# Optimization experiments

Measured on AMD Instinct MI355X. Metric: run time of the kernel, lower is better.

## Reference

```python
import jax, jax.numpy as jnp
import numpy as np

B, NI, D, P, R = 32, 1024, 1024, 1000, 3  # batch, patches, d_model, pool_size, agg rounds


def setup_inputs() -> dict:
    key = jax.random.key(0)
    ks = jax.random.split(key, 12)
    w = lambda k, shape: jax.random.normal(k, shape, jnp.float32) * 0.02
    return {
        "att_feats": jax.random.normal(ks[0], (B, NI, D), jnp.float32),
        "fc_feats": jax.random.normal(ks[1], (B, D), jnp.float32),
        "pool": jax.random.normal(ks[2], (P, D), jnp.float32),
        "W_agg": w(ks[3], (R, D, D)),          # stacked agg projections (no bias)
        "Wq": w(ks[4], (D, D)), "bq": jnp.zeros((D,), jnp.float32),
        "Wk": w(ks[5], (D, D)), "bk": jnp.zeros((D,), jnp.float32),
        "Wv": w(ks[6], (D, D)), "bv": jnp.zeros((D,), jnp.float32),
        "Wc": w(ks[7], (D, D)), "bc": jnp.zeros((D,), jnp.float32),
        "Wg": w(ks[8], (2 * D,)), "bg": jnp.asarray(-1.0, jnp.float32),  # gate bias init -1
        "residual_scale": jnp.asarray(0.1, jnp.float32),
    }


def reference(att_feats, fc_feats, pool, W_agg, Wq, bq, Wk, bk, Wv, bv, Wc, bc, Wg, bg, residual_scale):
    d = att_feats.shape[-1]
    scale = 1.0 / jnp.sqrt(jnp.asarray(d, att_feats.dtype))
    v_hat = fc_feats  # fc dim == d_model path

    # Aggregate attention: R rounds over normality pool, averaged (Eq. 4-6)
    q_all = jnp.einsum('bd,rod->rbo', v_hat, W_agg)            # [R,B,D]
    scores = jnp.einsum('rbo,po->rbp', q_all, pool) * scale    # [R,B,P]
    weights = jax.nn.softmax(scores, axis=-1)
    v_agg = jnp.einsum('rbp,pd->bd', weights, pool) / R        # [B,D]

    # Differentiate attention (Eq. 7-10)
    q = v_hat @ Wq.T + bq
    k = v_agg @ Wk.T + bk
    v = v_agg @ Wv.T + bv
    sim = jnp.sum(q * k, axis=-1, keepdims=True) * scale       # [B,1]
    v_common = jax.nn.sigmoid(sim) * v
    v_diff = jax.nn.relu((v_hat - v_common) @ Wc.T + bc)       # [B,D] (dropout = identity, eval)

    # Gated residual; split gate weight to avoid materializing the concat
    Wg1, Wg2 = Wg[:d], Wg[d:]
    g = jax.nn.sigmoid(att_feats @ Wg1 + (v_diff @ Wg2)[:, None] + bg)  # [B,NI]
    return att_feats + residual_scale * g[..., None] * v_diff[:, None, :]
```

## Files before the change

kernel.cpp:

```cpp
#include <hip/hip_runtime.h>

#define D 1024
#define B 32
#define NI 1024
#define PP 1000
#define R 3
#define SPLITS 8
#define VS 8
#define BK 32
#define KT (D / SPLITS / BK)
#define PAD 34

typedef float f32x4_t __attribute__((ext_vector_type(4)));

__device__ __forceinline__ void nt_store4(float* p, float4 v) {
    f32x4_t x = {v.x, v.y, v.z, v.w};
    __builtin_nontemporal_store(x, (f32x4_t*)p);
}

__device__ __forceinline__ float wred(float x) {
    #pragma unroll
    for (int off = 32; off; off >>= 1) x += __shfl_xor(x, off, 64);
    return x;
}
__device__ __forceinline__ float wmax(float x) {
    #pragma unroll
    for (int off = 32; off; off >>= 1) x = fmaxf(x, __shfl_xor(x, off, 64));
    return x;
}

template<int NXS>
__device__ __forceinline__ void gemm_core(
        const float* __restrict__ A, int mbase, int Mrows,
        const float* __restrict__ Xb, int xrstride, size_t xss,
        int kc0, float acc[4][4]) {
    __shared__ float Ws[128][PAD];
    __shared__ float Xs[32][PAD];
    const int t = threadIdx.x;
    const int ty = t >> 3, tx = t & 7;
    const int m0 = 4 * ty, b0 = 4 * tx;
    const int lrow = t >> 3, lq = t & 7;

    #pragma unroll
    for (int i = 0; i < 4; ++i)
        #pragma unroll
        for (int j = 0; j < 4; ++j) acc[i][j] = 0.f;

    for (int kt = 0; kt < KT; ++kt) {
        const int kc = kc0 + kt * BK;
        #pragma unroll
        for (int rr = 0; rr < 4; ++rr) {
            const int row = lrow + 32 * rr;
            float4 v = make_float4(0.f, 0.f, 0.f, 0.f);
            if (mbase + row < Mrows)
                v = *(const float4*)(A + (size_t)(mbase + row) * D + kc + 4 * lq);
            *(float2*)&Ws[row][4 * lq]     = make_float2(v.x, v.y);
            *(float2*)&Ws[row][4 * lq + 2] = make_float2(v.z, v.w);
        }
        {
            const float* xp = Xb + (size_t)lrow * xrstride + kc + 4 * lq;
            float4 v = *(const float4*)xp;
            #pragma unroll
            for (int s = 1; s < NXS; ++s) {
                float4 w = *(const float4*)(xp + (size_t)s * xss);
                v.x += w.x; v.y += w.y; v.z += w.z; v.w += w.w;
            }
            *(float2*)&Xs[lrow][4 * lq]     = make_float2(v.x, v.y);
            *(float2*)&Xs[lrow][4 * lq + 2] = make_float2(v.z, v.w);
        }
        __syncthreads();
        #pragma unroll
        for (int kp = 0; kp < 16; ++kp) {
            float2 wv[4], xv[4];
            #pragma unroll
            for (int i = 0; i < 4; ++i) wv[i] = *(const float2*)&Ws[m0 + i][2 * kp];
            #pragma unroll
            for (int j = 0; j < 4; ++j) xv[j] = *(const float2*)&Xs[b0 + j][2 * kp];
            #pragma unroll
            for (int i = 0; i < 4; ++i)
                #pragma unroll
                for (int j = 0; j < 4; ++j) {
                    acc[i][j] += wv[i].x * xv[j].x;
                    acc[i][j] += wv[i].y * xv[j].y;
                }
        }
        __syncthreads();
    }
}

__global__ __launch_bounds__(256) void gemm_k1(const float* __restrict__ Wagg,
        const float* __restrict__ fc, float* __restrict__ Cp) {
    const int mb = blockIdx.x, s = blockIdx.y;
    const int mbase = mb * 128;
    float acc[4][4];
    gemm_core<1>(Wagg, mbase, R * D, fc, D, 0, s * 128, acc);
    const int t = threadIdx.x, ty = t >> 3, tx = t & 7;
    const int m = mbase + 4 * ty;
    #pragma unroll
    for (int j = 0; j < 4; ++j) {
        float* cp = Cp + ((size_t)(s * B) + 4 * tx + j) * (R * D) + m;
        *(float4*)cp = make_float4(acc[0][j], acc[1][j], acc[2][j], acc[3][j]);
    }
}

__global__ __launch_bounds__(256) void gemm_k2(const float* __restrict__ pool,
        const float* __restrict__ qallp, float* __restrict__ Cp) {
    const int mb = blockIdx.x, s = blockIdx.y, r = blockIdx.z;
    const int mbase = mb * 128;
    float acc[4][4];
    gemm_core<SPLITS>(pool, mbase, PP, qallp + r * D, R * D, (size_t)B * R * D,
                      s * 128, acc);
    const int t = threadIdx.x, ty = t >> 3, tx = t & 7;
    const int m = mbase + 4 * ty;
    if (m >= PP) return;
    #pragma unroll
    for (int j = 0; j < 4; ++j) {
        float* cp = Cp + ((size_t)((s * R + r) * B) + 4 * tx + j) * D + m;
        *(float4*)cp = make_float4(acc[0][j], acc[1][j], acc[2][j], acc[3][j]);
    }
}

__global__ __launch_bounds__(256) void gemm_k5(const float* __restrict__ Wq,
        const float* __restrict__ Wk, const float* __restrict__ Wv,
        const float* __restrict__ fc, const float* __restrict__ vaggp,
        float* __restrict__ Cp) {
    const int mb = blockIdx.x, s = blockIdx.y, z = blockIdx.z;
    const int mbase = mb * 128;
    float acc[4][4];
    if (z == 0)
        gemm_core<1>(Wq, mbase, D, fc, D, 0, s * 128, acc);
    else
        gemm_core<VS>((z == 1) ? Wk : Wv, mbase, D, vaggp, D, (size_t)B * D,
                      s * 128, acc);
    const int t = threadIdx.x, ty = t >> 3, tx = t & 7;
    const int m = mbase + 4 * ty;
    #pragma unroll
    for (int j = 0; j < 4; ++j) {
        float* cp = Cp + ((size_t)((s * R + z) * B) + 4 * tx + j) * D + m;
        *(float4*)cp = make_float4(acc[0][j], acc[1][j], acc[2][j], acc[3][j]);
    }
}

__global__ __launch_bounds__(256) void gemm_k7(const float* __restrict__ Wc,
        const float* __restrict__ u, float* __restrict__ Cp) {
    const int mb = blockIdx.x, s = blockIdx.y;
    const int mbase = mb * 128;
    float acc[4][4];
    gemm_core<1>(Wc, mbase, D, u, D, 0, s * 128, acc);
    const int t = threadIdx.x, ty = t >> 3, tx = t & 7;
    const int m = mbase + 4 * ty;
    #pragma unroll
    for (int j = 0; j < 4; ++j) {
        float* cp = Cp + ((size_t)(s * B) + 4 * tx + j) * D + m;
        *(float4*)cp = make_float4(acc[0][j], acc[1][j], acc[2][j], acc[3][j]);
    }
}

__global__ __launch_bounds__(256) void k3_wbar(const float* __restrict__ scp,
        float* __restrict__ wbar) {
    const int b = blockIdx.x;
    const int t = threadIdx.x, w = t >> 6, lane = t & 63;
    __shared__ float red[8];
    float wb[4] = {0.f, 0.f, 0.f, 0.f};
    for (int r = 0; r < R; ++r) {
        float v[4];
        float mx = -1e30f;
        #pragma unroll
        for (int i = 0; i < 4; ++i) {
            const int p = t + 256 * i;
            float x = -1e30f;
            if (p < PP) {
                x = 0.f;
                #pragma unroll
                for (int s = 0; s < SPLITS; ++s)
                    x += scp[((size_t)((s * R + r) * B) + b) * D + p];
                x *= 0.03125f;
            }
            v[i] = x;
            mx = fmaxf(mx, x);
        }
        mx = wmax(mx);
        if (lane == 0) red[w] = mx;
        __syncthreads();
        mx = fmaxf(fmaxf(red[0], red[1]), fmaxf(red[2], red[3]));
        float e[4], sum = 0.f;
        #pragma unroll
        for (int i = 0; i < 4; ++i) {
            const int p = t + 256 * i;
            e[i] = (p < PP) ? __expf(v[i] - mx) : 0.f;
            sum += e[i];
        }
        sum = wred(sum);
        if (lane == 0) red[4 + w] = sum;
        __syncthreads();
        const float inv = 1.f / (red[4] + red[5] + red[6] + red[7]);
        #pragma unroll
        for (int i = 0; i < 4; ++i) wb[i] += e[i] * inv;
        __syncthreads();
    }
    #pragma unroll
    for (int i = 0; i < 4; ++i) {
        const int p = t + 256 * i;
        wbar[(size_t)b * 1024 + p] = wb[i] * (1.f / 3.f);
    }
}

__global__ __launch_bounds__(256) void k4_vagg(const float* __restrict__ wbar,
        const float* __restrict__ pool, float* __restrict__ vaggp) {
    const int db = blockIdx.x, ps = blockIdx.y;
    __shared__ float Ps[32][132];
    __shared__ float Wbt[32][36];
    const int t = threadIdx.x;
    const int ty = t >> 3, tx = t & 7;
    float acc[4][4];
    #pragma unroll
    for (int i = 0; i < 4; ++i)
        #pragma unroll
        for (int j = 0; j < 4; ++j) acc[i][j] = 0.f;

    for (int pt = 0; pt < 4; ++pt) {
        const int p0 = ps * 128 + pt * 32;
        {
            const int prow = t >> 5, qc = t & 31;
            #pragma unroll
            for (int rr = 0; rr < 4; ++rr) {
                const int pr = prow + 8 * rr;
                float4 v = make_float4(0.f, 0.f, 0.f, 0.f);
                if (p0 + pr < PP)
                    v = *(const float4*)(pool + (size_t)(p0 + pr) * D + db * 128 + 4 * qc);
                *(float4*)&Ps[pr][4 * qc] = v;
            }
        }
        {
            const int bb = t >> 3, q = t & 7;
            float4 v = *(const float4*)(wbar + (size_t)bb * 1024 + p0 + 4 * q);
            Wbt[4 * q + 0][bb] = v.x; Wbt[4 * q + 1][bb] = v.y;
            Wbt[4 * q + 2][bb] = v.z; Wbt[4 * q + 3][bb] = v.w;
        }
        __syncthreads();
        #pragma unroll
        for (int pg = 0; pg < 8; ++pg) {
            #pragma unroll
            for (int pp = 0; pp < 4; ++pp) {
                const int p = 4 * pg + pp;
                float4 xv = *(const float4*)&Ps[p][4 * ty];
                float4 wv = *(const float4*)&Wbt[p][4 * tx];
                const float xs[4] = {xv.x, xv.y, xv.z, xv.w};
                const float wsv[4] = {wv.x, wv.y, wv.z, wv.w};
                #pragma unroll
                for (int i = 0; i < 4; ++i)
                    #pragma unroll
                    for (int j = 0; j < 4; ++j)
                        acc[i][j] += xs[i] * wsv[j];
            }
        }
        __syncthreads();
    }
    const int dbase = db * 128 + 4 * ty;
    #pragma unroll
    for (int j = 0; j < 4; ++j) {
        float* op = vaggp + ((size_t)ps * B + 4 * tx + j) * D + dbase;
        *(float4*)op = make_float4(acc[0][j], acc[1][j], acc[2][j], acc[3][j]);
    }
}

__global__ __launch_bounds__(256) void k6_u(const float* __restrict__ qkvp,
        const float* __restrict__ bq, const float* __restrict__ bk,
        const float* __restrict__ bv, const float* __restrict__ vhat,
        float* __restrict__ u) {
    const int b = blockIdx.x;
    const int t = threadIdx.x, w = t >> 6, lane = t & 63;
    const int d = 4 * t;
    float4 qv = *(const float4*)(bq + d);
    float4 kv = *(const float4*)(bk + d);
    #pragma unroll
    for (int s = 0; s < SPLITS; ++s) {
        float4 a = *(const float4*)(qkvp + ((size_t)((s * R + 0) * B) + b) * D + d);
        float4 c = *(const float4*)(qkvp + ((size_t)((s * R + 1) * B) + b) * D + d);
        qv.x += a.x; qv.y += a.y; qv.z += a.z; qv.w += a.w;
        kv.x += c.x; kv.y += c.y; kv.z += c.z; kv.w += c.w;
    }
    float local = qv.x * kv.x + qv.y * kv.y + qv.z * kv.z + qv.w * kv.w;
    local = wred(local);
    __shared__ float red[4];
    if (lane == 0) red[w] = local;
    __syncthreads();
    const float sim = (red[0] + red[1] + red[2] + red[3]) * 0.03125f;
    const float sig = 1.f / (1.f + __expf(-sim));
    float4 vv = *(const float4*)(bv + d);
    #pragma unroll
    for (int s = 0; s < SPLITS; ++s) {
        float4 c = *(const float4*)(qkvp + ((size_t)((s * R + 2) * B) + b) * D + d);
        vv.x += c.x; vv.y += c.y; vv.z += c.z; vv.w += c.w;
    }
    const float4 vh = *(const float4*)(vhat + (size_t)b * D + d);
    float4 o;
    o.x = vh.x - sig * vv.x; o.y = vh.y - sig * vv.y;
    o.z = vh.z - sig * vv.z; o.w = vh.w - sig * vv.w;
    *(float4*)(u + (size_t)b * D + d) = o;
}

__global__ __launch_bounds__(256) void k8_cb(const float* __restrict__ vdp,
        const float* __restrict__ bc, const float* __restrict__ Wg,
        const float* __restrict__ bg, float* __restrict__ vdiff,
        float* __restrict__ cb) {
    const int b = blockIdx.x;
    const int t = threadIdx.x, w = t >> 6, lane = t & 63;
    const int d = 4 * t;
    float4 a = *(const float4*)(bc + d);
    #pragma unroll
    for (int s = 0; s < SPLITS; ++s) {
        float4 c = *(const float4*)(vdp + ((size_t)(s * B) + b) * D + d);
        a.x += c.x; a.y += c.y; a.z += c.z; a.w += c.w;
    }
    a.x = fmaxf(a.x, 0.f); a.y = fmaxf(a.y, 0.f);
    a.z = fmaxf(a.z, 0.f); a.w = fmaxf(a.w, 0.f);
    *(float4*)(vdiff + (size_t)b * D + d) = a;
    const float4 g2 = *(const float4*)(Wg + D + d);
    float local = a.x * g2.x + a.y * g2.y + a.z * g2.z + a.w * g2.w;
    local = wred(local);
    __shared__ float red[4];
    if (lane == 0) red[w] = local;
    __syncthreads();
    if (t == 0) cb[b] = red[0] + red[1] + red[2] + red[3] + bg[0];
}

__global__ __launch_bounds__(256, 2) void k9_main(const float* __restrict__ att,
        const float* __restrict__ Wg, const float* __restrict__ cb,
        const float* __restrict__ vdiff, const float* __restrict__ rs_p,
        float* __restrict__ out) {
    __shared__ float vds[1024];
    const int t = threadIdx.x;
    const int b = blockIdx.x >> 5;
    *(float4*)&vds[4 * t] = *(const float4*)(vdiff + (size_t)b * D + 4 * t);
    __syncthreads();
    const int w = t >> 6, lane = t & 63;
    float4 g[4];
    #pragma unroll
    for (int kk = 0; kk < 4; ++kk)
        g[kk] = *(const float4*)(Wg + 4 * lane + 256 * kk);
    const float rsv = rs_p[0];
    const float cbb = cb[b];
    const size_t row0 = (size_t)b * NI + (size_t)(blockIdx.x & 31) * 32 + w * 8;
    const float* ap = att + row0 * D;
    float* op = out + row0 * D;

    float4 cur[8], nxt[8];
    #pragma unroll
    for (int q = 0; q < 8; ++q)
        cur[q] = *(const float4*)(ap + (size_t)(q >> 2) * D + 4 * lane + 256 * (q & 3));

    #pragma unroll
    for (int it = 0; it < 4; ++it) {
        if (it < 3) {
            const float* apn = ap + (size_t)(2 * it + 2) * D;
            #pragma unroll
            for (int q = 0; q < 8; ++q)
                nxt[q] = *(const float4*)(apn + (size_t)(q >> 2) * D + 4 * lane + 256 * (q & 3));
        }
        float acc0 = 0.f, acc1 = 0.f;
        #pragma unroll
        for (int kk = 0; kk < 4; ++kk) {
            acc0 += cur[kk].x * g[kk].x + cur[kk].y * g[kk].y +
                    cur[kk].z * g[kk].z + cur[kk].w * g[kk].w;
            acc1 += cur[4 + kk].x * g[kk].x + cur[4 + kk].y * g[kk].y +
                    cur[4 + kk].z * g[kk].z + cur[4 + kk].w * g[kk].w;
        }
        #pragma unroll
        for (int off = 32; off; off >>= 1) {
            acc0 += __shfl_xor(acc0, off, 64);
            acc1 += __shfl_xor(acc1, off, 64);
        }
        const float grs0 = rsv / (1.f + __expf(-(acc0 + cbb)));
        const float grs1 = rsv / (1.f + __expf(-(acc1 + cbb)));
        float* op0 = op + (size_t)(2 * it) * D;
        #pragma unroll
        for (int kk = 0; kk < 4; ++kk) {
            const int col = 4 * lane + 256 * kk;
            const float4 vd = *(const float4*)&vds[col];
            float4 o0, o1;
            o0.x = cur[kk].x + grs0 * vd.x; o0.y = cur[kk].y + grs0 * vd.y;
            o0.z = cur[kk].z + grs0 * vd.z; o0.w = cur[kk].w + grs0 * vd.w;
            o1.x = cur[4 + kk].x + grs1 * vd.x; o1.y = cur[4 + kk].y + grs1 * vd.y;
            o1.z = cur[4 + kk].z + grs1 * vd.z; o1.w = cur[4 + kk].w + grs1 * vd.w;
            nt_store4(op0 + col, o0);
            nt_store4(op0 + D + col, o1);
        }
        if (it < 3) {
            #pragma unroll
            for (int q = 0; q < 8; ++q) cur[q] = nxt[q];
        }
    }
}

extern "C" void kernel_launch(void* const* d_in, const int* in_sizes, int n_in,
                              void* d_out, int out_size, void* d_ws, size_t ws_size,
                              hipStream_t stream) {
    const float* att  = (const float*)d_in[0];
    const float* fc   = (const float*)d_in[1];
    const float* pool = (const float*)d_in[2];
    const float* Wagg = (const float*)d_in[3];
    const float* Wq   = (const float*)d_in[4];
    const float* bq   = (const float*)d_in[5];
    const float* Wk   = (const float*)d_in[6];
    const float* bk   = (const float*)d_in[7];
    const float* Wv   = (const float*)d_in[8];
    const float* bv   = (const float*)d_in[9];
    const float* Wc   = (const float*)d_in[10];
    const float* bc   = (const float*)d_in[11];
    const float* Wg   = (const float*)d_in[12];
    const float* bg   = (const float*)d_in[13];
    const float* rs   = (const float*)d_in[14];
    float* out = (float*)d_out;

    float* ws = (float*)d_ws;
    float* qallp = ws;
    float* scp   = qallp + (size_t)SPLITS * B * R * D;
    float* wbar  = scp + (size_t)SPLITS * R * B * D;
    float* vaggp = wbar + (size_t)B * 1024;
    float* qkvp  = vaggp + (size_t)VS * B * D;
    float* ub    = qkvp + (size_t)SPLITS * R * B * D;
    float* vdp   = ub + (size_t)B * D;
    float* vdiff = vdp + (size_t)SPLITS * B * D;
    float* cbuf  = vdiff + (size_t)B * D;

    gemm_k1<<<dim3(24, SPLITS), 256, 0, stream>>>(Wagg, fc, qallp);
    gemm_k2<<<dim3(8, SPLITS, R), 256, 0, stream>>>(pool, qallp, scp);
    k3_wbar<<<B, 256, 0, stream>>>(scp, wbar);
    k4_vagg<<<dim3(8, VS), 256, 0, stream>>>(wbar, pool, vaggp);
    gemm_k5<<<dim3(8, SPLITS, R), 256, 0, stream>>>(Wq, Wk, Wv, fc, vaggp, qkvp);
    k6_u<<<B, 256, 0, stream>>>(qkvp, bq, bk, bv, fc, ub);
    gemm_k7<<<dim3(8, SPLITS), 256, 0, stream>>>(Wc, ub, vdp);
    k8_cb<<<B, 256, 0, stream>>>(vdp, bc, Wg, bg, vdiff, cbuf);
    k9_main<<<B * 32, 256, 0, stream>>>(att, Wg, cbuf, vdiff, rs, out);
}
```

Before: 131.2 us.

## Fuse eight dependent small kernels into one cooperative kernel with grid syncs

Replaces the chain of eight small GEMM and reduction launches with a single cooperative kernel of 192 blocks that runs each stage in turn, separated by grid-wide barriers. It also moves the Wq projection so it runs alongside the v_agg stage, since the two do not depend on each other. The aim is to remove per-launch overhead and the gaps between dependent launches. The cost is grid.sync barriers, idle blocks in the narrow stages, and a fixed grid size that must fit co-resident on the device.

```diff
diff --git a/kernel.cpp b/kernel.cpp
--- a/kernel.cpp
+++ b/kernel.cpp
@@ -1,4 +1,7 @@
 #include <hip/hip_runtime.h>
+#include <hip/hip_cooperative_groups.h>
+
+namespace cg = cooperative_groups;
 
 #define D 1024
 #define B 32
@@ -30,12 +33,10 @@
 }
 
 template<int NXS>
-__device__ __forceinline__ void gemm_core(
+__device__ __forceinline__ void gemm_core_l(
         const float* __restrict__ A, int mbase, int Mrows,
         const float* __restrict__ Xb, int xrstride, size_t xss,
-        int kc0, float acc[4][4]) {
-    __shared__ float Ws[128][PAD];
-    __shared__ float Xs[32][PAD];
+        int kc0, float acc[4][4], float (*Ws)[PAD], float (*Xs)[PAD]) {
     const int t = threadIdx.x;
     const int ty = t >> 3, tx = t & 7;
     const int m0 = 4 * ty, b0 = 4 * tx;
@@ -88,241 +89,252 @@
     }
 }
 
-__global__ __launch_bounds__(256) void gemm_k1(const float* __restrict__ Wagg,
-        const float* __restrict__ fc, float* __restrict__ Cp) {
-    const int mb = blockIdx.x, s = blockIdx.y;
-    const int mbase = mb * 128;
-    float acc[4][4];
-    gemm_core<1>(Wagg, mbase, R * D, fc, D, 0, s * 128, acc);
-    const int t = threadIdx.x, ty = t >> 3, tx = t & 7;
-    const int m = mbase + 4 * ty;
-    #pragma unroll
-    for (int j = 0; j < 4; ++j) {
-        float* cp = Cp + ((size_t)(s * B) + 4 * tx + j) * (R * D) + m;
-        *(float4*)cp = make_float4(acc[0][j], acc[1][j], acc[2][j], acc[3][j]);
-    }
-}
-
-__global__ __launch_bounds__(256) void gemm_k2(const float* __restrict__ pool,
-        const float* __restrict__ qallp, float* __restrict__ Cp) {
-    const int mb = blockIdx.x, s = blockIdx.y, r = blockIdx.z;
-    const int mbase = mb * 128;
-    float acc[4][4];
-    gemm_core<SPLITS>(pool, mbase, PP, qallp + r * D, R * D, (size_t)B * R * D,
-                      s * 128, acc);
-    const int t = threadIdx.x, ty = t >> 3, tx = t & 7;
-    const int m = mbase + 4 * ty;
-    if (m >= PP) return;
-    #pragma unroll
-    for (int j = 0; j < 4; ++j) {
-        float* cp = Cp + ((size_t)((s * R + r) * B) + 4 * tx + j) * D + m;
-        *(float4*)cp = make_float4(acc[0][j], acc[1][j], acc[2][j], acc[3][j]);
-    }
-}
-
-__global__ __launch_bounds__(256) void gemm_k5(const float* __restrict__ Wq,
+__global__ __launch_bounds__(256) void chain_all(
+        const float* __restrict__ fc, const float* __restrict__ pool,
+        const float* __restrict__ Wagg, const float* __restrict__ Wq,
         const float* __restrict__ Wk, const float* __restrict__ Wv,
-        const float* __restrict__ fc, const float* __restrict__ vaggp,
-        float* __restrict__ Cp) {
-    const int mb = blockIdx.x, s = blockIdx.y, z = blockIdx.z;
-    const int mbase = mb * 128;
-    float acc[4][4];
-    if (z == 0)
-        gemm_core<1>(Wq, mbase, D, fc, D, 0, s * 128, acc);
-    else
-        gemm_core<VS>((z == 1) ? Wk : Wv, mbase, D, vaggp, D, (size_t)B * D,
-                      s * 128, acc);
-    const int t = threadIdx.x, ty = t >> 3, tx = t & 7;
-    const int m = mbase + 4 * ty;
-    #pragma unroll
-    for (int j = 0; j < 4; ++j) {
-        float* cp = Cp + ((size_t)((s * R + z) * B) + 4 * tx + j) * D + m;
-        *(float4*)cp = make_float4(acc[0][j], acc[1][j], acc[2][j], acc[3][j]);
-    }
-}
-
-__global__ __launch_bounds__(256) void gemm_k7(const float* __restrict__ Wc,
-        const float* __restrict__ u, float* __restrict__ Cp) {
-    const int mb = blockIdx.x, s = blockIdx.y;
-    const int mbase = mb * 128;
-    float acc[4][4];
-    gemm_core<1>(Wc, mbase, D, u, D, 0, s * 128, acc);
-    const int t = threadIdx.x, ty = t >> 3, tx = t & 7;
-    const int m = mbase + 4 * ty;
-    #pragma unroll
-    for (int j = 0; j < 4; ++j) {
-        float* cp = Cp + ((size_t)(s * B) + 4 * tx + j) * D + m;
-        *(float4*)cp = make_float4(acc[0][j], acc[1][j], acc[2][j], acc[3][j]);
-    }
-}
-
-__global__ __launch_bounds__(256) void k3_wbar(const float* __restrict__ scp,
-        float* __restrict__ wbar) {
-    const int b = blockIdx.x;
-    const int t = threadIdx.x, w = t >> 6, lane = t & 63;
-    __shared__ float red[8];
-    float wb[4] = {0.f, 0.f, 0.f, 0.f};
-    for (int r = 0; r < R; ++r) {
-        float v[4];
-        float mx = -1e30f;
-        #pragma unroll
-        for (int i = 0; i < 4; ++i) {
-            const int p = t + 256 * i;
-            float x = -1e30f;
-            if (p < PP) {
-                x = 0.f;
+        const float* __restrict__ bq, const float* __restrict__ bk,
+        const float* __restrict__ bv, const float* __restrict__ Wc,
+        const float* __restrict__ bc, const float* __restrict__ Wg,
+        const float* __restrict__ bg,
+        float* __restrict__ qallp, float* __restrict__ scp,
+        float* __restrict__ wbar, float* __restrict__ vaggp,
+        float* __restrict__ qkvp, float* __restrict__ ub,
+        float* __restrict__ vdp, float* __restrict__ vdiff,
+        float* __restrict__ cb) {
+    cg::grid_group grid = cg::this_grid();
+    const int bid = blockIdx.x;
+    const int t = threadIdx.x;
+    __shared__ float lds_raw[160 * PAD];
+    __shared__ float red8[8];
+    float (*Ws)[PAD] = (float(*)[PAD])lds_raw;
+    float (*Xs)[PAD] = (float(*)[PAD])&lds_raw[128 * PAD];
+    const int ty = t >> 3, tx = t & 7;
+
+    {
+        const int mb = bid / SPLITS, s = bid % SPLITS;
+        float acc[4][4];
+        gemm_core_l<1>(Wagg, mb * 128, R * D, fc, D, 0, s * 128, acc, Ws, Xs);
+        const int m = mb * 128 + 4 * ty;
+        #pragma unroll
+        for (int j = 0; j < 4; ++j) {
+            float* cp = qallp + ((size_t)(s * B) + 4 * tx + j) * (R * D) + m;
+            *(float4*)cp = make_float4(acc[0][j], acc[1][j], acc[2][j], acc[3][j]);
+        }
+    }
+    grid.sync();
+
+    {
+        const int r = bid / 64, rem = bid % 64;
+        const int s = rem >> 3, mb = rem & 7;
+        float acc[4][4];
+        gemm_core_l<SPLITS>(pool, mb * 128, PP, qallp + r * D, R * D,
+                            (size_t)B * R * D, s * 128, acc, Ws, Xs);
+        const int m = mb * 128 + 4 * ty;
+        if (m < PP) {
+            #pragma unroll
+            for (int j = 0; j < 4; ++j) {
+                float* cp = scp + ((size_t)((s * R + r) * B) + 4 * tx + j) * D + m;
+                *(float4*)cp = make_float4(acc[0][j], acc[1][j], acc[2][j], acc[3][j]);
+            }
+        }
+    }
+    grid.sync();
+
+    if (bid < B) {
+        const int b = bid;
+        const int w = t >> 6, lane = t & 63;
+        float wb[4] = {0.f, 0.f, 0.f, 0.f};
+        for (int r = 0; r < R; ++r) {
+            float v[4];
+            float mx = -1e30f;
+            #pragma unroll
+            for (int i = 0; i < 4; ++i) {
+                const int p = t + 256 * i;
+                float x = -1e30f;
+                if (p < PP) {
+                    x = 0.f;
+                    #pragma unroll
+                    for (int s = 0; s < SPLITS; ++s)
+                        x += scp[((size_t)((s * R + r) * B) + b) * D + p];
+                    x *= 0.03125f;
+                }
+                v[i] = x;
+                mx = fmaxf(mx, x);
+            }
+            mx = wmax(mx);
+            if (lane == 0) red8[w] = mx;
+            __syncthreads();
+            mx = fmaxf(fmaxf(red8[0], red8[1]), fmaxf(red8[2], red8[3]));
+            float e[4], sum = 0.f;
+            #pragma unroll
+            for (int i = 0; i < 4; ++i) {
+                const int p = t + 256 * i;
+                e[i] = (p < PP) ? __expf(v[i] - mx) : 0.f;
+                sum += e[i];
+            }
+            sum = wred(sum);
+            if (lane == 0) red8[4 + w] = sum;
+            __syncthreads();
+            const float inv = 1.f / (red8[4] + red8[5] + red8[6] + red8[7]);
+            #pragma unroll
+            for (int i = 0; i < 4; ++i) wb[i] += e[i] * inv;
+            __syncthreads();
+        }
+        #pragma unroll
+        for (int i = 0; i < 4; ++i)
+            wbar[(size_t)b * 1024 + t + 256 * i] = wb[i] * (1.f / 3.f);
+    }
+    grid.sync();
+
+    if (bid < 64) {
+        const int db = bid & 7, ps = bid >> 3;
+        float (*Ps)[132] = (float(*)[132])lds_raw;
+        float (*Wbt)[36] = (float(*)[36])&lds_raw[32 * 132];
+        float acc[4][4];
+        #pragma unroll
+        for (int i = 0; i < 4; ++i)
+            #pragma unroll
+            for (int j = 0; j < 4; ++j) acc[i][j] = 0.f;
+        for (int pt = 0; pt < 4; ++pt) {
+            const int p0 = ps * 128 + pt * 32;
+            {
+                const int prow = t >> 5, qc = t & 31;
                 #pragma unroll
-                for (int s = 0; s < SPLITS; ++s)
-                    x += scp[((size_t)((s * R + r) * B) + b) * D + p];
-                x *= 0.03125f;
-            }
-            v[i] = x;
-            mx = fmaxf(mx, x);
-        }
-        mx = wmax(mx);
-        if (lane == 0) red[w] = mx;
+                for (int rr = 0; rr < 4; ++rr) {
+                    const int pr = prow + 8 * rr;
+                    float4 v = make_float4(0.f, 0.f, 0.f, 0.f);
+                    if (p0 + pr < PP)
+                        v = *(const float4*)(pool + (size_t)(p0 + pr) * D + db * 128 + 4 * qc);
+                    *(float4*)&Ps[pr][4 * qc] = v;
+                }
+            }
+            {
+                const int bb = t >> 3, q = t & 7;
+                float4 v = *(const float4*)(wbar + (size_t)bb * 1024 + p0 + 4 * q);
+                Wbt[4 * q + 0][bb] = v.x; Wbt[4 * q + 1][bb] = v.y;
+                Wbt[4 * q + 2][bb] = v.z; Wbt[4 * q + 3][bb] = v.w;
+            }
+            __syncthreads();
+            #pragma unroll
+            for (int pg = 0; pg < 8; ++pg) {
+                #pragma unroll
+                for (int pp = 0; pp < 4; ++pp) {
+                    const int p = 4 * pg + pp;
+                    float4 xv = *(const float4*)&Ps[p][4 * ty];
+                    float4 wv = *(const float4*)&Wbt[p][4 * tx];
+                    const float xsv[4] = {xv.x, xv.y, xv.z, xv.w};
+                    const float wsv[4] = {wv.x, wv.y, wv.z, wv.w};
+                    #pragma unroll
+                    for (int i = 0; i < 4; ++i)
+                        #pragma unroll
+                        for (int j = 0; j < 4; ++j)
+                            acc[i][j] += xsv[i] * wsv[j];
+                }
+            }
+            __syncthreads();
+        }
+        const int dbase = db * 128 + 4 * ty;
+        #pragma unroll
+        for (int j = 0; j < 4; ++j) {
+            float* op = vaggp + ((size_t)ps * B + 4 * tx + j) * D + dbase;
+            *(float4*)op = make_float4(acc[0][j], acc[1][j], acc[2][j], acc[3][j]);
+        }
+    } else if (bid < 128) {
+        const int i0 = bid - 64;
+        const int mb = i0 & 7, s = i0 >> 3;
+        float acc[4][4];
+        gemm_core_l<1>(Wq, mb * 128, D, fc, D, 0, s * 128, acc, Ws, Xs);
+        const int m = mb * 128 + 4 * ty;
+        #pragma unroll
+        for (int j = 0; j < 4; ++j) {
+            float* cp = qkvp + ((size_t)((s * R + 0) * B) + 4 * tx + j) * D + m;
+            *(float4*)cp = make_float4(acc[0][j], acc[1][j], acc[2][j], acc[3][j]);
+        }
+    }
+    grid.sync();
+
+    if (bid < 128) {
+        const int z = bid >> 6, rem = bid & 63;
+        const int s = rem >> 3, mb = rem & 7;
+        float acc[4][4];
+        gemm_core_l<VS>((z == 0) ? Wk : Wv, mb * 128, D, vaggp, D,
+                        (size_t)B * D, s * 128, acc, Ws, Xs);
+        const int m = mb * 128 + 4 * ty;
+        #pragma unroll
+        for (int j = 0; j < 4; ++j) {
+            float* cp = qkvp + ((size_t)((s * R + z + 1) * B) + 4 * tx + j) * D + m;
+            *(float4*)cp = make_float4(acc[0][j], acc[1][j], acc[2][j], acc[3][j]);
+        }
+    }
+    grid.sync();
+
+    if (bid < B) {
+        const int b = bid;
+        const int w = t >> 6, lane = t & 63;
+        const int d = 4 * t;
+        float4 qv = *(const float4*)(bq + d);
+        float4 kv = *(const float4*)(bk + d);
+        #pragma unroll
+        for (int s = 0; s < SPLITS; ++s) {
+            float4 a = *(const float4*)(qkvp + ((size_t)((s * R + 0) * B) + b) * D + d);
+            float4 c = *(const float4*)(qkvp + ((size_t)((s * R + 1) * B) + b) * D + d);
+            qv.x += a.x; qv.y += a.y; qv.z += a.z; qv.w += a.w;
+            kv.x += c.x; kv.y += c.y; kv.z += c.z; kv.w += c.w;
+        }
+        float local = qv.x * kv.x + qv.y * kv.y + qv.z * kv.z + qv.w * kv.w;
+        local = wred(local);
+        if (lane == 0) red8[w] = local;
         __syncthreads();
-        mx = fmaxf(fmaxf(red[0], red[1]), fmaxf(red[2], red[3]));
-        float e[4], sum = 0.f;
-        #pragma unroll
-        for (int i = 0; i < 4; ++i) {
-            const int p = t + 256 * i;
-            e[i] = (p < PP) ? __expf(v[i] - mx) : 0.f;
-            sum += e[i];
-        }
-        sum = wred(sum);
-        if (lane == 0) red[4 + w] = sum;
+        const float sim = (red8[0] + red8[1] + red8[2] + red8[3]) * 0.03125f;
+        const float sig = 1.f / (1.f + __expf(-sim));
+        float4 vv = *(const float4*)(bv + d);
+        #pragma unroll
+        for (int s = 0; s < SPLITS; ++s) {
+            float4 c = *(const float4*)(qkvp + ((size_t)((s * R + 2) * B) + b) * D + d);
+            vv.x += c.x; vv.y += c.y; vv.z += c.z; vv.w += c.w;
+        }
+        const float4 vh = *(const float4*)(fc + (size_t)b * D + d);
+        float4 o;
+        o.x = vh.x - sig * vv.x; o.y = vh.y - sig * vv.y;
+        o.z = vh.z - sig * vv.z; o.w = vh.w - sig * vv.w;
+        *(float4*)(ub + (size_t)b * D + d) = o;
+    }
+    grid.sync();
+
+    if (bid < 64) {
+        const int s = bid >> 3, mb = bid & 7;
+        float acc[4][4];
+        gemm_core_l<1>(Wc, mb * 128, D, ub, D, 0, s * 128, acc, Ws, Xs);
+        const int m = mb * 128 + 4 * ty;
+        #pragma unroll
+        for (int j = 0; j < 4; ++j) {
+            float* cp = vdp + ((size_t)(s * B) + 4 * tx + j) * D + m;
+            *(float4*)cp = make_float4(acc[0][j], acc[1][j], acc[2][j], acc[3][j]);
+        }
+    }
+    grid.sync();
+
+    if (bid < B) {
+        const int b = bid;
+        const int w = t >> 6, lane = t & 63;
+        const int d = 4 * t;
+        float4 a = *(const float4*)(bc + d);
+        #pragma unroll
+        for (int s = 0; s < SPLITS; ++s) {
+            float4 c = *(const float4*)(vdp + ((size_t)(s * B) + b) * D + d);
+            a.x += c.x; a.y += c.y; a.z += c.z; a.w += c.w;
+        }
+        a.x = fmaxf(a.x, 0.f); a.y = fmaxf(a.y, 0.f);
+        a.z = fmaxf(a.z, 0.f); a.w = fmaxf(a.w, 0.f);
+        *(float4*)(vdiff + (size_t)b * D + d) = a;
+        const float4 g2 = *(const float4*)(Wg + D + d);
+        float local = a.x * g2.x + a.y * g2.y + a.z * g2.z + a.w * g2.w;
+        local = wred(local);
+        if (lane == 0) red8[w] = local;
         __syncthreads();
-        const float inv = 1.f / (red[4] + red[5] + red[6] + red[7]);
-        #pragma unroll
-        for (int i = 0; i < 4; ++i) wb[i] += e[i] * inv;
-        __syncthreads();
-    }
-    #pragma unroll
-    for (int i = 0; i < 4; ++i) {
-        const int p = t + 256 * i;
-        wbar[(size_t)b * 1024 + p] = wb[i] * (1.f / 3.f);
-    }
-}
-
-__global__ __launch_bounds__(256) void k4_vagg(const float* __restrict__ wbar,
-        const float* __restrict__ pool, float* __restrict__ vaggp) {
-    const int db = blockIdx.x, ps = blockIdx.y;
-    __shared__ float Ps[32][132];
-    __shared__ float Wbt[32][36];
-    const int t = threadIdx.x;
-    const int ty = t >> 3, tx = t & 7;
-    float acc[4][4];
-    #pragma unroll
-    for (int i = 0; i < 4; ++i)
-        #pragma unroll
-        for (int j = 0; j < 4; ++j) acc[i][j] = 0.f;
-
-    for (int pt = 0; pt < 4; ++pt) {
-        const int p0 = ps * 128 + pt * 32;
-        {
-            const int prow = t >> 5, qc = t & 31;
-            #pragma unroll
-            for (int rr = 0; rr < 4; ++rr) {
-                const int pr = prow + 8 * rr;
-                float4 v = make_float4(0.f, 0.f, 0.f, 0.f);
-                if (p0 + pr < PP)
-                    v = *(const float4*)(pool + (size_t)(p0 + pr) * D + db * 128 + 4 * qc);
-                *(float4*)&Ps[pr][4 * qc] = v;
-            }
-        }
-        {
-            const int bb = t >> 3, q = t & 7;
-            float4 v = *(const float4*)(wbar + (size_t)bb * 1024 + p0 + 4 * q);
-            Wbt[4 * q + 0][bb] = v.x; Wbt[4 * q + 1][bb] = v.y;
-            Wbt[4 * q + 2][bb] = v.z; Wbt[4 * q + 3][bb] = v.w;
-        }
-        __syncthreads();
-        #pragma unroll
-        for (int pg = 0; pg < 8; ++pg) {
-            #pragma unroll
-            for (int pp = 0; pp < 4; ++pp) {
-                const int p = 4 * pg + pp;
-                float4 xv = *(const float4*)&Ps[p][4 * ty];
-                float4 wv = *(const float4*)&Wbt[p][4 * tx];
-                const float xs[4] = {xv.x, xv.y, xv.z, xv.w};
-                const float wsv[4] = {wv.x, wv.y, wv.z, wv.w};
-                #pragma unroll
-                for (int i = 0; i < 4; ++i)
-                    #pragma unroll
-                    for (int j = 0; j < 4; ++j)
-                        acc[i][j] += xs[i] * wsv[j];
-            }
-        }
-        __syncthreads();
-    }
-    const int dbase = db * 128 + 4 * ty;
-    #pragma unroll
-    for (int j = 0; j < 4; ++j) {
-        float* op = vaggp + ((size_t)ps * B + 4 * tx + j) * D + dbase;
-        *(float4*)op = make_float4(acc[0][j], acc[1][j], acc[2][j], acc[3][j]);
-    }
-}
-
-__global__ __launch_bounds__(256) void k6_u(const float* __restrict__ qkvp,
-        const float* __restrict__ bq, const float* __restrict__ bk,
-        const float* __restrict__ bv, const float* __restrict__ vhat,
-        float* __restrict__ u) {
-    const int b = blockIdx.x;
-    const int t = threadIdx.x, w = t >> 6, lane = t & 63;
-    const int d = 4 * t;
-    float4 qv = *(const float4*)(bq + d);
-    float4 kv = *(const float4*)(bk + d);
-    #pragma unroll
-    for (int s = 0; s < SPLITS; ++s) {
-        float4 a = *(const float4*)(qkvp + ((size_t)((s * R + 0) * B) + b) * D + d);
-        float4 c = *(const float4*)(qkvp + ((size_t)((s * R + 1) * B) + b) * D + d);
-        qv.x += a.x; qv.y += a.y; qv.z += a.z; qv.w += a.w;
-        kv.x += c.x; kv.y += c.y; kv.z += c.z; kv.w += c.w;
-    }
-    float local = qv.x * kv.x + qv.y * kv.y + qv.z * kv.z + qv.w * kv.w;
-    local = wred(local);
-    __shared__ float red[4];
-    if (lane == 0) red[w] = local;
-    __syncthreads();
-    const float sim = (red[0] + red[1] + red[2] + red[3]) * 0.03125f;
-    const float sig = 1.f / (1.f + __expf(-sim));
-    float4 vv = *(const float4*)(bv + d);
-    #pragma unroll
-    for (int s = 0; s < SPLITS; ++s) {
-        float4 c = *(const float4*)(qkvp + ((size_t)((s * R + 2) * B) + b) * D + d);
-        vv.x += c.x; vv.y += c.y; vv.z += c.z; vv.w += c.w;
-    }
-    const float4 vh = *(const float4*)(vhat + (size_t)b * D + d);
-    float4 o;
-    o.x = vh.x - sig * vv.x; o.y = vh.y - sig * vv.y;
-    o.z = vh.z - sig * vv.z; o.w = vh.w - sig * vv.w;
-    *(float4*)(u + (size_t)b * D + d) = o;
-}
-
-__global__ __launch_bounds__(256) void k8_cb(const float* __restrict__ vdp,
-        const float* __restrict__ bc, const float* __restrict__ Wg,
-        const float* __restrict__ bg, float* __restrict__ vdiff,
-        float* __restrict__ cb) {
-    const int b = blockIdx.x;
-    const int t = threadIdx.x, w = t >> 6, lane = t & 63;
-    const int d = 4 * t;
-    float4 a = *(const float4*)(bc + d);
-    #pragma unroll
-    for (int s = 0; s < SPLITS; ++s) {
-        float4 c = *(const float4*)(vdp + ((size_t)(s * B) + b) * D + d);
-        a.x += c.x; a.y += c.y; a.z += c.z; a.w += c.w;
-    }
-    a.x = fmaxf(a.x, 0.f); a.y = fmaxf(a.y, 0.f);
-    a.z = fmaxf(a.z, 0.f); a.w = fmaxf(a.w, 0.f);
-    *(float4*)(vdiff + (size_t)b * D + d) = a;
-    const float4 g2 = *(const float4*)(Wg + D + d);
-    float local = a.x * g2.x + a.y * g2.y + a.z * g2.z + a.w * g2.w;
-    local = wred(local);
-    __shared__ float red[4];
-    if (lane == 0) red[w] = local;
-    __syncthreads();
-    if (t == 0) cb[b] = red[0] + red[1] + red[2] + red[3] + bg[0];
+        if (t == 0) cb[b] = red8[0] + red8[1] + red8[2] + red8[3] + bg[0];
+    }
 }
 
 __global__ __launch_bounds__(256, 2) void k9_main(const float* __restrict__ att,
@@ -424,13 +436,14 @@
     float* vdiff = vdp + (size_t)SPLITS * B * D;
     float* cbuf  = vdiff + (size_t)B * D;
 
-    gemm_k1<<<dim3(24, SPLITS), 256, 0, stream>>>(Wagg, fc, qallp);
-    gemm_k2<<<dim3(8, SPLITS, R), 256, 0, stream>>>(pool, qallp, scp);
-    k3_wbar<<<B, 256, 0, stream>>>(scp, wbar);
-    k4_vagg<<<dim3(8, VS), 256, 0, stream>>>(wbar, pool, vaggp);
-    gemm_k5<<<dim3(8, SPLITS, R), 256, 0, stream>>>(Wq, Wk, Wv, fc, vaggp, qkvp);
-    k6_u<<<B, 256, 0, stream>>>(qkvp, bq, bk, bv, fc, ub);
-    gemm_k7<<<dim3(8, SPLITS), 256, 0, stream>>>(Wc, ub, vdp);
-    k8_cb<<<B, 256, 0, stream>>>(vdp, bc, Wg, bg, vdiff, cbuf);
+    void* args[] = {
+        (void*)&fc, (void*)&pool, (void*)&Wagg, (void*)&Wq, (void*)&Wk,
+        (void*)&Wv, (void*)&bq, (void*)&bk, (void*)&bv, (void*)&Wc,
+        (void*)&bc, (void*)&Wg, (void*)&bg,
+        (void*)&qallp, (void*)&scp, (void*)&wbar, (void*)&vaggp,
+        (void*)&qkvp, (void*)&ub, (void*)&vdp, (void*)&vdiff, (void*)&cbuf
+    };
+    hipLaunchCooperativeKernel((void*)chain_all, dim3(192), dim3(256),
+                               args, 0, stream);
     k9_main<<<B * 32, 256, 0, stream>>>(att, Wg, cbuf, vdiff, rs, out);
 }
```

Result: slower. 294.1 us (+124.1%).

## Move Wq projection into first GEMM and hand-pipeline gated residual loads

Applied to the files above, without the earlier changes.

The Wq·fc projection does not depend on the aggregation result, so it moves from the K/V GEMM launch into the first Wagg GEMM launch as extra blocks. The K/V GEMM shrinks to two z-slices, which shortens the serial chain of small kernels. The main streaming kernel now issues its att loads as inline-asm dwordx4 loads into double buffers, with explicit vmcnt waits and sched barriers so loads of the next row pair overlap compute and stores of the current pair. Its min-blocks launch bound is also dropped. The explicit waitcnt counting relies on the nontemporal stores not being counted against vmcnt in a way that breaks ordering, and dropping the occupancy hint may change register allocation.

```diff
diff --git a/kernel.cpp b/kernel.cpp
--- a/kernel.cpp
+++ b/kernel.cpp
@@ -13,8 +13,7 @@
 
 typedef float f32x4_t __attribute__((ext_vector_type(4)));
 
-__device__ __forceinline__ void nt_store4(float* p, float4 v) {
-    f32x4_t x = {v.x, v.y, v.z, v.w};
+__device__ __forceinline__ void nt_store4v(float* p, f32x4_t x) {
     __builtin_nontemporal_store(x, (f32x4_t*)p);
 }
 
@@ -88,18 +87,30 @@
     }
 }
 
-__global__ __launch_bounds__(256) void gemm_k1(const float* __restrict__ Wagg,
-        const float* __restrict__ fc, float* __restrict__ Cp) {
+__global__ __launch_bounds__(256) void gemm_k1q(const float* __restrict__ Wagg,
+        const float* __restrict__ Wq, const float* __restrict__ fc,
+        float* __restrict__ qallp, float* __restrict__ qkvp) {
     const int mb = blockIdx.x, s = blockIdx.y;
-    const int mbase = mb * 128;
+    const int t = threadIdx.x, ty = t >> 3, tx = t & 7;
     float acc[4][4];
-    gemm_core<1>(Wagg, mbase, R * D, fc, D, 0, s * 128, acc);
-    const int t = threadIdx.x, ty = t >> 3, tx = t & 7;
-    const int m = mbase + 4 * ty;
-    #pragma unroll
-    for (int j = 0; j < 4; ++j) {
-        float* cp = Cp + ((size_t)(s * B) + 4 * tx + j) * (R * D) + m;
-        *(float4*)cp = make_float4(acc[0][j], acc[1][j], acc[2][j], acc[3][j]);
+    if (mb < 24) {
+        const int mbase = mb * 128;
+        gemm_core<1>(Wagg, mbase, R * D, fc, D, 0, s * 128, acc);
+        const int m = mbase + 4 * ty;
+        #pragma unroll
+        for (int j = 0; j < 4; ++j) {
+            float* cp = qallp + ((size_t)(s * B) + 4 * tx + j) * (R * D) + m;
+            *(float4*)cp = make_float4(acc[0][j], acc[1][j], acc[2][j], acc[3][j]);
+        }
+    } else {
+        const int mbase = (mb - 24) * 128;
+        gemm_core<1>(Wq, mbase, D, fc, D, 0, s * 128, acc);
+        const int m = mbase + 4 * ty;
+        #pragma unroll
+        for (int j = 0; j < 4; ++j) {
+            float* cp = qkvp + ((size_t)((s * R + 0) * B) + 4 * tx + j) * D + m;
+            *(float4*)cp = make_float4(acc[0][j], acc[1][j], acc[2][j], acc[3][j]);
+        }
     }
 }
 
@@ -120,23 +131,19 @@
     }
 }
 
-__global__ __launch_bounds__(256) void gemm_k5(const float* __restrict__ Wq,
-        const float* __restrict__ Wk, const float* __restrict__ Wv,
-        const float* __restrict__ fc, const float* __restrict__ vaggp,
+__global__ __launch_bounds__(256) void gemm_k5kv(const float* __restrict__ Wk,
+        const float* __restrict__ Wv, const float* __restrict__ vaggp,
         float* __restrict__ Cp) {
     const int mb = blockIdx.x, s = blockIdx.y, z = blockIdx.z;
     const int mbase = mb * 128;
     float acc[4][4];
-    if (z == 0)
-        gemm_core<1>(Wq, mbase, D, fc, D, 0, s * 128, acc);
-    else
-        gemm_core<VS>((z == 1) ? Wk : Wv, mbase, D, vaggp, D, (size_t)B * D,
-                      s * 128, acc);
+    gemm_core<VS>((z == 0) ? Wk : Wv, mbase, D, vaggp, D, (size_t)B * D,
+                  s * 128, acc);
     const int t = threadIdx.x, ty = t >> 3, tx = t & 7;
     const int m = mbase + 4 * ty;
     #pragma unroll
     for (int j = 0; j < 4; ++j) {
-        float* cp = Cp + ((size_t)((s * R + z) * B) + 4 * tx + j) * D + m;
+        float* cp = Cp + ((size_t)((s * R + z + 1) * B) + 4 * tx + j) * D + m;
         *(float4*)cp = make_float4(acc[0][j], acc[1][j], acc[2][j], acc[3][j]);
     }
 }
@@ -325,7 +332,10 @@
     if (t == 0) cb[b] = red[0] + red[1] + red[2] + red[3] + bg[0];
 }
 
-__global__ __launch_bounds__(256, 2) void k9_main(const float* __restrict__ att,
+#define LD16(dst, srcp) \
+    asm volatile("global_load_dwordx4 %0, %1, off" : "=v"(dst) : "v"(srcp) : "memory")
+
+__global__ __launch_bounds__(256) void k9_main(const float* __restrict__ att,
         const float* __restrict__ Wg, const float* __restrict__ cb,
         const float* __restrict__ vdiff, const float* __restrict__ rs_p,
         float* __restrict__ out) {
@@ -341,56 +351,71 @@
         g[kk] = *(const float4*)(Wg + 4 * lane + 256 * kk);
     const float rsv = rs_p[0];
     const float cbb = cb[b];
-    const size_t row0 = (size_t)b * NI + (size_t)(blockIdx.x & 31) * 32 + w * 8;
+    const size_t row0 = (size_t)blockIdx.x * 32 + w * 8;
     const float* ap = att + row0 * D;
     float* op = out + row0 * D;
-
-    float4 cur[8], nxt[8];
-    #pragma unroll
-    for (int q = 0; q < 8; ++q)
-        cur[q] = *(const float4*)(ap + (size_t)(q >> 2) * D + 4 * lane + 256 * (q & 3));
-
-    #pragma unroll
-    for (int it = 0; it < 4; ++it) {
-        if (it < 3) {
-            const float* apn = ap + (size_t)(2 * it + 2) * D;
-            #pragma unroll
-            for (int q = 0; q < 8; ++q)
-                nxt[q] = *(const float4*)(apn + (size_t)(q >> 2) * D + 4 * lane + 256 * (q & 3));
-        }
-        float acc0 = 0.f, acc1 = 0.f;
-        #pragma unroll
-        for (int kk = 0; kk < 4; ++kk) {
-            acc0 += cur[kk].x * g[kk].x + cur[kk].y * g[kk].y +
-                    cur[kk].z * g[kk].z + cur[kk].w * g[kk].w;
-            acc1 += cur[4 + kk].x * g[kk].x + cur[4 + kk].y * g[kk].y +
-                    cur[4 + kk].z * g[kk].z + cur[4 + kk].w * g[kk].w;
-        }
-        #pragma unroll
-        for (int off = 32; off; off >>= 1) {
-            acc0 += __shfl_xor(acc0, off, 64);
-            acc1 += __shfl_xor(acc1, off, 64);
-        }
-        const float grs0 = rsv / (1.f + __expf(-(acc0 + cbb)));
-        const float grs1 = rsv / (1.f + __expf(-(acc1 + cbb)));
-        float* op0 = op + (size_t)(2 * it) * D;
-        #pragma unroll
-        for (int kk = 0; kk < 4; ++kk) {
-            const int col = 4 * lane + 256 * kk;
-            const float4 vd = *(const float4*)&vds[col];
-            float4 o0, o1;
-            o0.x = cur[kk].x + grs0 * vd.x; o0.y = cur[kk].y + grs0 * vd.y;
-            o0.z = cur[kk].z + grs0 * vd.z; o0.w = cur[kk].w + grs0 * vd.w;
-            o1.x = cur[4 + kk].x + grs1 * vd.x; o1.y = cur[4 + kk].y + grs1 * vd.y;
-            o1.z = cur[4 + kk].z + grs1 * vd.z; o1.w = cur[4 + kk].w + grs1 * vd.w;
-            nt_store4(op0 + col, o0);
-            nt_store4(op0 + D + col, o1);
-        }
-        if (it < 3) {
-            #pragma unroll
-            for (int q = 0; q < 8; ++q) cur[q] = nxt[q];
-        }
-    }
+    const int co = 4 * lane;
+
+    f32x4_t bufA[8], bufB[8];
+
+#define PAIR_COMPUTE_STORE(BUF, OPB)                                          \
+    {                                                                         \
+        float acc0 = 0.f, acc1 = 0.f;                                         \
+        _Pragma("unroll")                                                     \
+        for (int kk = 0; kk < 4; ++kk) {                                      \
+            acc0 += BUF[kk][0] * g[kk].x + BUF[kk][1] * g[kk].y +             \
+                    BUF[kk][2] * g[kk].z + BUF[kk][3] * g[kk].w;              \
+            acc1 += BUF[4 + kk][0] * g[kk].x + BUF[4 + kk][1] * g[kk].y +     \
+                    BUF[4 + kk][2] * g[kk].z + BUF[4 + kk][3] * g[kk].w;      \
+        }                                                                     \
+        _Pragma("unroll")                                                     \
+        for (int off = 32; off; off >>= 1) {                                  \
+            acc0 += __shfl_xor(acc0, off, 64);                                \
+            acc1 += __shfl_xor(acc1, off, 64);                                \
+        }                                                                     \
+        const float grs0 = rsv / (1.f + __expf(-(acc0 + cbb)));               \
+        const float grs1 = rsv / (1.f + __expf(-(acc1 + cbb)));               \
+        _Pragma("unroll")                                                     \
+        for (int kk = 0; kk < 4; ++kk) {                                      \
+            const int col = co + 256 * kk;                                    \
+            const float4 vd = *(const float4*)&vds[col];                      \
+            f32x4_t o0, o1;                                                   \
+            o0[0] = BUF[kk][0] + grs0 * vd.x; o0[1] = BUF[kk][1] + grs0 * vd.y; \
+            o0[2] = BUF[kk][2] + grs0 * vd.z; o0[3] = BUF[kk][3] + grs0 * vd.w; \
+            o1[0] = BUF[4 + kk][0] + grs1 * vd.x; o1[1] = BUF[4 + kk][1] + grs1 * vd.y; \
+            o1[2] = BUF[4 + kk][2] + grs1 * vd.z; o1[3] = BUF[4 + kk][3] + grs1 * vd.w; \
+            nt_store4v((OPB) + col, o0);                                      \
+            nt_store4v((OPB) + D + col, o1);                                  \
+        }                                                                     \
+    }
+
+#define ISSUE_PAIR(BUF, ROWOFF)                                               \
+    _Pragma("unroll")                                                         \
+    for (int q = 0; q < 8; ++q) {                                             \
+        const float* _src = ap + (size_t)((ROWOFF) + (q >> 2)) * D + co + 256 * (q & 3); \
+        LD16(BUF[q], _src);                                                   \
+    }
+
+    ISSUE_PAIR(bufA, 0);
+    asm volatile("s_waitcnt vmcnt(0)");
+    __builtin_amdgcn_sched_barrier(0);
+
+    ISSUE_PAIR(bufB, 2);
+    PAIR_COMPUTE_STORE(bufA, op);
+
+    ISSUE_PAIR(bufA, 4);
+    asm volatile("s_waitcnt vmcnt(16)");
+    __builtin_amdgcn_sched_barrier(0);
+    PAIR_COMPUTE_STORE(bufB, op + 2 * D);
+
+    ISSUE_PAIR(bufB, 6);
+    asm volatile("s_waitcnt vmcnt(16)");
+    __builtin_amdgcn_sched_barrier(0);
+    PAIR_COMPUTE_STORE(bufA, op + 4 * D);
+
+    asm volatile("s_waitcnt vmcnt(8)");
+    __builtin_amdgcn_sched_barrier(0);
+    PAIR_COMPUTE_STORE(bufB, op + 6 * D);
 }
 
 extern "C" void kernel_launch(void* const* d_in, const int* in_sizes, int n_in,
@@ -424,11 +449,11 @@
     float* vdiff = vdp + (size_t)SPLITS * B * D;
     float* cbuf  = vdiff + (size_t)B * D;
 
-    gemm_k1<<<dim3(24, SPLITS), 256, 0, stream>>>(Wagg, fc, qallp);
+    gemm_k1q<<<dim3(32, SPLITS), 256, 0, stream>>>(Wagg, Wq, fc, qallp, qkvp);
     gemm_k2<<<dim3(8, SPLITS, R), 256, 0, stream>>>(pool, qallp, scp);
     k3_wbar<<<B, 256, 0, stream>>>(scp, wbar);
     k4_vagg<<<dim3(8, VS), 256, 0, stream>>>(wbar, pool, vaggp);
-    gemm_k5<<<dim3(8, SPLITS, R), 256, 0, stream>>>(Wq, Wk, Wv, fc, vaggp, qkvp);
+    gemm_k5kv<<<dim3(8, SPLITS, 2), 256, 0, stream>>>(Wk, Wv, vaggp, qkvp);
     k6_u<<<B, 256, 0, stream>>>(qkvp, bq, bk, bv, fc, ub);
     gemm_k7<<<dim3(8, SPLITS), 256, 0, stream>>>(Wc, ub, vdp);
     k8_cb<<<B, 256, 0, stream>>>(vdp, bc, Wg, bg, vdiff, cbuf);
```

Measured after the change: 129.8 us. No clear change (-1.1%).
